# Performance work log

Hardware: AMD Instinct MI355X
Metric: run time of the kernel (lower is better)

## Reference

```python
import jax, jax.numpy as jnp
import numpy as np

N, C, H, W = 4, 256, 32, 32
NH = 2                      # att_nhead
HD = C // NH                # 128 per-head dim
MAX_DIS = 7
WS = 2 * MAX_DIS + 1        # 15 window side
WW = WS * WS                # 225 window positions
T = (C / NH) ** 0.5


def _gather_idx(h, w):
    # idx[wpos, m]: flat index into zero-padded (h+14, w+14) grid of the
    # neighbor at window offset wpos for query pixel m (== F.unfold semantics)
    pw = w + 2 * MAX_DIS
    dy, dx = np.meshgrid(np.arange(WS), np.arange(WS), indexing='ij')
    ys, xs = np.meshgrid(np.arange(h), np.arange(w), indexing='ij')
    idx = (dy.reshape(-1, 1) + ys.reshape(1, -1)) * pw + (dx.reshape(-1, 1) + xs.reshape(1, -1))
    return jnp.asarray(idx, dtype=jnp.int32)  # [WW, h*w]


def setup_inputs() -> dict:
    key = jax.random.key(0)
    ks = jax.random.split(key, 14)
    s = 0.02
    return {
        'q': jax.random.normal(ks[0], (N, C, H, W), jnp.float32),
        'k': jax.random.normal(ks[1], (N, C, H, W), jnp.float32),
        'v': jax.random.normal(ks[2], (N, C, H, W), jnp.float32),
        'Wq': jax.random.normal(ks[3], (C, C), jnp.float32) * s,
        'bq': jnp.zeros((C,), jnp.float32),
        'Wk': jax.random.normal(ks[4], (C, C), jnp.float32) * s,
        'bk': jnp.zeros((C,), jnp.float32),
        'Wv': jax.random.normal(ks[5], (C, C), jnp.float32) * s,
        'bv': jnp.zeros((C,), jnp.float32),
        'Wrel': jax.random.normal(ks[6], (NH, WW, HD), jnp.float32) * s,   # grouped 1x1 conv
        'brel': jnp.zeros((NH * WW,), jnp.float32),
        'V_bias': jax.random.normal(ks[7], (NH, HD, WW), jnp.float32) * s,
        'Wfc': jax.random.normal(ks[8], (C, C), jnp.float32) * s,
        'bfc': jnp.zeros((C,), jnp.float32),
    }


def _conv1x1(x, Wt, b):
    return jnp.einsum('nchw,dc->ndhw', x, Wt) + b[None, :, None, None]


def reference(q, k, v, Wq, bq, Wk, bk, Wv, bv, Wrel, brel, V_bias, Wfc, bfc):
    n, c, h, w = q.shape
    hw = h * w
    idx = _gather_idx(h, w)                                   # [WW, hw]
    pad = ((0, 0), (0, 0), (0, 0), (MAX_DIS, MAX_DIS), (MAX_DIS, MAX_DIS))

    q = _conv1x1(q, Wq, bq)
    k = _conv1x1(k, Wk, bk)
    v = _conv1x1(v, Wv, bv)

    # grouped 1x1 conv: relative position logits, [n, NH, WW, hw]
    rel = jnp.einsum('ngcxy,gwc->ngwxy', q.reshape(n, NH, HD, h, w), Wrel)
    rel = rel + brel.reshape(NH, WW)[None, :, :, None, None]
    rel = rel.reshape(n, NH, WW, hw)

    qs = (q / T).reshape(n, NH, HD, hw)

    # unfold K via zero-pad + gather: [n, NH, HD, WW, hw]
    k_pad = jnp.pad(k.reshape(n, NH, HD, h, w), pad).reshape(n, NH, HD, -1)
    k_un = k_pad[..., idx]
    qk = jnp.einsum('ngcm,ngcwm->ngwm', qs, k_un) + rel

    # boundary mask: neighbor inside the original image
    valid = jnp.pad(jnp.ones((h, w), jnp.float32), MAX_DIS).reshape(-1)[idx] > 0
    qk = jnp.where(valid[None, None], qk, jnp.float32(-1e8))
    attn = jax.nn.softmax(qk, axis=2)                         # over window positions

    agg_bias = jnp.einsum('ngwm,gcw->mngc', attn, V_bias).reshape(hw, n, c)

    # local2global scatter + dense einsum == gather of zero-padded V
    v_pad = jnp.pad(v.reshape(n, NH, HD, h, w), pad).reshape(n, NH, HD, -1)
    v_un = v_pad[..., idx]                                    # [n, NH, HD, WW, hw]
    agg_value = jnp.einsum('ngwm,ngcwm->mngc', attn, v_un).reshape(hw, n, c)

    out = (agg_value + agg_bias) @ Wfc.T + bfc                # [hw, n, c]
    return out
```

## Files before the change

### kernel.cpp

```cpp
#include <hip/hip_runtime.h>
#include <math.h>


typedef __attribute__((ext_vector_type(8))) short short8;
typedef __attribute__((ext_vector_type(4))) short short4v;
typedef __attribute__((ext_vector_type(4))) float floatx4;

__device__ __forceinline__ short f2bf(float f) {
    unsigned u = __float_as_uint(f);
    unsigned r = (u + 0x7fffu + ((u >> 16) & 1u)) >> 16;
    return (short)r;
}
__device__ __forceinline__ float bf2f(short s) {
    return __uint_as_float(((unsigned)(unsigned short)s) << 16);
}

__global__ __launch_bounds__(64)
void conv_w(const float* __restrict__ Wq, const float* __restrict__ Wk,
            const float* __restrict__ Wv, const float* __restrict__ Wfc,
            const float* __restrict__ Wrel, const float* __restrict__ Vb,
            short* __restrict__ Whi, short* __restrict__ Wlo,
            short* __restrict__ Wrh, short* __restrict__ Wrl,
            short* __restrict__ Vbh, short* __restrict__ Vbl)
{
    const int lane = threadIdx.x;
    const int n16 = lane & 15, quad = lane >> 4;
    const int z = blockIdx.z;

    if (z < 4) {
        const float* W = (z == 0 ? Wq : z == 1 ? Wk : z == 2 ? Wv : Wfc);
        const int dt = blockIdx.x, kc = blockIdx.y;
        const int d = dt * 16 + n16, cb = kc * 32 + quad * 8;
        float4 w0 = *(const float4*)&W[d * 256 + cb];
        float4 w1 = *(const float4*)&W[d * 256 + cb + 4];
        float f[8] = {w0.x, w0.y, w0.z, w0.w, w1.x, w1.y, w1.z, w1.w};
        short8 h8, l8;
#pragma unroll
        for (int j = 0; j < 8; ++j) {
            short hb = f2bf(f[j]);
            h8[j] = hb;
            l8[j] = f2bf(f[j] - bf2f(hb));
        }
        long off = (long)z * 65536 + (((long)(dt * 8 + kc) * 64) + lane) * 8;
        *(short8*)(Whi + off) = h8;
        *(short8*)(Wlo + off) = l8;
    } else if (z < 6) {
        const int g = z - 4;
        const int wt = blockIdx.x, kc = blockIdx.y;
        if (wt >= 15 || kc >= 4) return;
        const int w = wt * 16 + n16;
        const int cb = kc * 32 + quad * 8;
        float f[8] = {0.f, 0.f, 0.f, 0.f, 0.f, 0.f, 0.f, 0.f};
        if (w < 225) {
            float4 w0 = *(const float4*)&Wrel[(long)(g * 225 + w) * 128 + cb];
            float4 w1 = *(const float4*)&Wrel[(long)(g * 225 + w) * 128 + cb + 4];
            f[0] = w0.x; f[1] = w0.y; f[2] = w0.z; f[3] = w0.w;
            f[4] = w1.x; f[5] = w1.y; f[6] = w1.z; f[7] = w1.w;
        }
        short8 h8, l8;
#pragma unroll
        for (int j = 0; j < 8; ++j) {
            short hb = f2bf(f[j]);
            h8[j] = hb;
            l8[j] = f2bf(f[j] - bf2f(hb));
        }
        long off = (long)g * 30720 + (((long)(wt * 4 + kc) * 64) + lane) * 8;
        *(short8*)(Wrh + off) = h8;
        *(short8*)(Wrl + off) = l8;
    } else {
        const int g = z - 6;
        const int dt = blockIdx.x, wk = blockIdx.y;
        if (dt >= 8) return;
        const int ch = dt * 16 + n16;
        const int w0 = wk * 32 + quad * 8;
        float f[8];
#pragma unroll
        for (int j = 0; j < 8; ++j) {
            int w = w0 + j;
            f[j] = (w < 225) ? Vb[(long)(g * 128 + ch) * 225 + w] : 0.f;
        }
        short8 h8, l8;
#pragma unroll
        for (int j = 0; j < 8; ++j) {
            short hb = f2bf(f[j]);
            h8[j] = hb;
            l8[j] = f2bf(f[j] - bf2f(hb));
        }
        long off = (((long)(g * 128 + ch)) << 8) + w0;
        *(short8*)(Vbh + off) = h8;
        *(short8*)(Vbl + off) = l8;
    }
}

__global__ __launch_bounds__(256)
void mfma_proj(const float* __restrict__ q, const float* __restrict__ k,
               const float* __restrict__ v,
               const short* __restrict__ Whi, const short* __restrict__ Wlo,
               const float* __restrict__ bq, const float* __restrict__ bk,
               const float* __restrict__ bv,
               short* __restrict__ qhi, short* __restrict__ qlo,
               short* __restrict__ khi, short* __restrict__ klo,
               short* __restrict__ vhi, short* __restrict__ vlo)
{
    __shared__ float st[256 * 17];
    const int tid = threadIdx.x;
    const int wave = tid >> 6, lane = tid & 63;
    const int n16 = lane & 15, quad = lane >> 4;
    const int mt16 = blockIdx.x, z = blockIdx.y;
    const int sel = z >> 2, batch = z & 3;

    const float* X = (sel == 0 ? q : sel == 1 ? k : v) + ((long)batch << 18);

    {
        const float* src = X + ((long)tid << 10) + mt16 * 16;
        float4 a0 = *(const float4*)(src);
        float4 a1 = *(const float4*)(src + 4);
        float4 a2 = *(const float4*)(src + 8);
        float4 a3 = *(const float4*)(src + 12);
        float* d = &st[tid * 17];
        d[0] = a0.x; d[1] = a0.y; d[2] = a0.z; d[3] = a0.w;
        d[4] = a1.x; d[5] = a1.y; d[6] = a1.z; d[7] = a1.w;
        d[8] = a2.x; d[9] = a2.y; d[10] = a2.z; d[11] = a2.w;
        d[12] = a3.x; d[13] = a3.y; d[14] = a3.z; d[15] = a3.w;
    }

    const float* bias = (sel == 0 ? bq : sel == 1 ? bk : bv);
    float bbv[4][4];
#pragma unroll
    for (int i = 0; i < 4; ++i) {
        float4 b4 = *(const float4*)&bias[(wave * 4 + i) * 16 + quad * 4];
        bbv[i][0] = b4.x; bbv[i][1] = b4.y; bbv[i][2] = b4.z; bbv[i][3] = b4.w;
    }
    __syncthreads();

    floatx4 acc[4] = {{0.f,0.f,0.f,0.f},{0.f,0.f,0.f,0.f},
                      {0.f,0.f,0.f,0.f},{0.f,0.f,0.f,0.f}};
    const long abase = (long)sel * 65536 + (long)lane * 8;
#pragma unroll
    for (int kc = 0; kc < 8; ++kc) {
        short8 bh, bl;
        const float* col = &st[(kc * 32 + quad * 8) * 17 + n16];
#pragma unroll
        for (int j = 0; j < 8; ++j) {
            float f = col[j * 17];
            short hb = f2bf(f);
            bh[j] = hb;
            bl[j] = f2bf(f - bf2f(hb));
        }
#pragma unroll
        for (int i = 0; i < 4; ++i) {
            const int dt = wave * 4 + i;
            short8 ahi = *(const short8*)(Whi + abase + (long)(dt * 8 + kc) * 512);
            short8 alo = *(const short8*)(Wlo + abase + (long)(dt * 8 + kc) * 512);
            acc[i] = __builtin_amdgcn_mfma_f32_16x16x32_bf16(ahi, bh, acc[i], 0, 0, 0);
            acc[i] = __builtin_amdgcn_mfma_f32_16x16x32_bf16(ahi, bl, acc[i], 0, 0, 0);
            acc[i] = __builtin_amdgcn_mfma_f32_16x16x32_bf16(alo, bh, acc[i], 0, 0, 0);
        }
    }

    if (sel == 2) {
        const int m = mt16 * 16 + n16;
        const int yq = m >> 5, col = (m & 31) + 8;
#pragma unroll
        for (int i = 0; i < 4; ++i) {
            const int dt = wave * 4 + i;
#pragma unroll
            for (int r = 0; r < 4; ++r) {
                const int ch = dt * 16 + quad * 4 + r;
                const int gg = ch >> 7, chh = ch & 127;
                float f = acc[i][r] + bbv[i][r];
                short hb = f2bf(f);
                short lb = f2bf(f - bf2f(hb));
                long o = (((long)((batch * 2 + gg) * 128 + chh) * 32 + yq)) * 48 + col;
                vhi[o] = hb;
                vlo[o] = lb;
            }
        }
        {
            const int prow = mt16 >> 1, side = mt16 & 1;
            const int gg = tid >> 7, chp = tid & 127;
            long po = (((long)((batch * 2 + gg) * 128 + chp) * 32 + prow)) * 48 + side * 40;
            short8 zz = {0,0,0,0,0,0,0,0};
            *(short8*)(vhi + po) = zz;
            *(short8*)(vlo + po) = zz;
        }
        return;
    }

    __syncthreads();
    float* tile = st;
#pragma unroll
    for (int i = 0; i < 4; ++i) {
        const int dt = wave * 4 + i;
#pragma unroll
        for (int r = 0; r < 4; ++r)
            tile[n16 * 257 + dt * 16 + quad * 4 + r] = acc[i][r] + bbv[i][r];
    }
    __syncthreads();

    const float scale = (sel == 1) ? 0.08838834764831845f : 1.0f;
    const int m_l = tid >> 4, c16 = (tid & 15) * 16;
    const int m = mt16 * 16 + m_l;
    short* oh = sel ? khi : qhi;
    short* ol = sel ? klo : qlo;
#pragma unroll
    for (int half = 0; half < 2; ++half) {
        const int cg = c16 + half * 8;
        short8 h8, l8;
#pragma unroll
        for (int j = 0; j < 8; ++j) {
            float f = tile[m_l * 257 + cg + j] * scale;
            short hb = f2bf(f);
            h8[j] = hb;
            l8[j] = f2bf(f - bf2f(hb));
        }
        const int g = cg >> 7, ch = cg & 127;
        const long base = (((long)(batch * 2 + g) << 10) + m) * 128 + ch;
        *(short8*)(oh + base) = h8;
        *(short8*)(ol + base) = l8;
    }
}

__global__ __launch_bounds__(256)
void scores_pv(const short* __restrict__ qhi, const short* __restrict__ qlo,
               const short* __restrict__ khi, const short* __restrict__ klo,
               const short* __restrict__ Wrh, const short* __restrict__ Wrl,
               const float* __restrict__ brel,
               const short* __restrict__ vhi, const short* __restrict__ vlo,
               const short* __restrict__ Vbh, const short* __restrict__ Vbl,
               short* __restrict__ AGhi, short* __restrict__ AGlo)
{
    __shared__ __align__(16) float qk[16 * 241];
    __shared__ __align__(16) short pah[16 * 264];
    __shared__ __align__(16) short pal[16 * 264];
    __shared__ float invl[16];

    const int tid = threadIdx.x;
    const int wave = tid >> 6, lane = tid & 63;
    const int lin = blockIdx.x;
    const int bz  = lin & 7;
    const int yy  = lin >> 3;
    const int y   = yy >> 1;
    const int xt  = yy & 1;
    const int g = bz & 1;
    const int x0 = xt * 16;

    const int n16 = lane & 15, quad = lane >> 4;
    const long qbase = (((long)bz << 10) + y * 32 + x0 + n16) * 128 + quad * 8;
    short8 a_hi[4], a_lo[4];
#pragma unroll
    for (int ch = 0; ch < 4; ++ch) {
        a_hi[ch] = *(const short8*)(qhi + qbase + ch * 32);
        a_lo[ch] = *(const short8*)(qlo + qbase + ch * 32);
    }

    for (int wt = wave; wt < 15; wt += 4) {
        const short* Ah = Wrh + (long)g * 30720 + ((long)(wt * 4) * 64 + lane) * 8;
        const short* Al = Wrl + (long)g * 30720 + ((long)(wt * 4) * 64 + lane) * 8;
        floatx4 racc = {0.f, 0.f, 0.f, 0.f};
#pragma unroll
        for (int kc = 0; kc < 4; ++kc) {
            short8 whh = *(const short8*)(Ah + kc * 512);
            short8 wll = *(const short8*)(Al + kc * 512);
            racc = __builtin_amdgcn_mfma_f32_16x16x32_bf16(whh, a_hi[kc], racc, 0, 0, 0);
            racc = __builtin_amdgcn_mfma_f32_16x16x32_bf16(whh, a_lo[kc], racc, 0, 0, 0);
            racc = __builtin_amdgcn_mfma_f32_16x16x32_bf16(wll, a_hi[kc], racc, 0, 0, 0);
        }
#pragma unroll
        for (int r = 0; r < 4; ++r) {
            int w = wt * 16 + quad * 4 + r;
            if (w < 225) {
                int dy = w / 15, dx = w - dy * 15;
                qk[n16 * 241 + dy * 16 + dx] = racc[r] + brel[g * 225 + w];
            }
        }
    }
    __syncthreads();

    for (int e = tid; e < 16 * 241; e += 256) {
        int px = e / 241, idx = e - px * 241;
        int dy = idx >> 4, dx = idx & 15;
        int hy = y + dy - 7, hx = x0 + px + dx - 7;
        bool valid = (dx < 15) && (dy < 15) &&
                     (hy >= 0) && (hy < 32) && (hx >= 0) && (hx < 32);
        if (!valid) qk[e] = -1e8f;
    }
    __syncthreads();

    for (int dy = wave; dy < 15; dy += 4) {
        const int ky = y + dy - 7;
        if (ky < 0 || ky > 31) continue;
#pragma unroll
        for (int kxt = 0; kxt < 2; ++kxt) {
            const int kxg = x0 - 8 + kxt * 16 + n16;
            const long kb = (((long)bz << 10) + ky * 32 + kxg) * 128 + quad * 8;
            floatx4 acc = {0.f, 0.f, 0.f, 0.f};
#pragma unroll
            for (int ch = 0; ch < 4; ++ch) {
                short8 b_hi = *(const short8*)(khi + kb + ch * 32);
                short8 b_lo = *(const short8*)(klo + kb + ch * 32);
                acc = __builtin_amdgcn_mfma_f32_16x16x32_bf16(a_hi[ch], b_hi, acc, 0, 0, 0);
                acc = __builtin_amdgcn_mfma_f32_16x16x32_bf16(a_hi[ch], b_lo, acc, 0, 0, 0);
                acc = __builtin_amdgcn_mfma_f32_16x16x32_bf16(a_lo[ch], b_hi, acc, 0, 0, 0);
            }
            if (kxg >= 0 && kxg < 32) {
#pragma unroll
                for (int r = 0; r < 4; ++r) {
                    int m = quad * 4 + r;
                    int dx = kxg - (x0 + m) + 7;
                    if (dx >= 0 && dx < 15) {
                        int s = m * 241 + dy * 16 + dx;
                        qk[s] = qk[s] + acc[r];
                    }
                }
            }
        }
    }
    __syncthreads();

    {
        int px = tid >> 4, s = tid & 15;
        float mx = -3.0e38f;
        for (int w = s; w < 240; w += 16) mx = fmaxf(mx, qk[px * 241 + w]);
#pragma unroll
        for (int msk = 8; msk; msk >>= 1) mx = fmaxf(mx, __shfl_xor(mx, msk));
        float sum = 0.f;
        for (int w = s; w < 240; w += 16) {
            float p = __expf(qk[px * 241 + w] - mx);
            qk[px * 241 + w] = p;
            sum += p;
        }
#pragma unroll
        for (int msk = 8; msk; msk >>= 1) sum += __shfl_xor(sum, msk);
        if (s == 0) invl[px] = 1.0f / sum;
    }
    __syncthreads();

    for (int e = tid; e < 4096; e += 256) {
        int px = e >> 8, w = e & 255;
        float p = 0.f;
        if (w < 225) {
            int dy2 = w / 15, dx2 = w - dy2 * 15;
            p = qk[px * 241 + dy2 * 16 + dx2] * invl[px];
        }
        short hb = f2bf(p);
        pah[px * 264 + w] = hb;
        pal[px * 264 + w] = f2bf(p - bf2f(hb));
    }
    __syncthreads();

    floatx4 acc[2] = {{0.f,0.f,0.f,0.f},{0.f,0.f,0.f,0.f}};
    const int ch0a = (wave * 2) * 16;
    const int ch0b = (wave * 2 + 1) * 16;

#pragma unroll
    for (int wk = 0; wk < 8; ++wk) {
        short8 pa_h = *(const short8*)&pah[n16 * 264 + wk * 32 + quad * 8];
        short8 pa_l = *(const short8*)&pal[n16 * 264 + wk * 32 + quad * 8];
        const long vb0 = (((long)(g * 128 + ch0a + n16)) << 8) + wk * 32 + quad * 8;
        const long vb1 = (((long)(g * 128 + ch0b + n16)) << 8) + wk * 32 + quad * 8;
        short8 b0h = *(const short8*)(Vbh + vb0);
        short8 b0l = *(const short8*)(Vbl + vb0);
        short8 b1h = *(const short8*)(Vbh + vb1);
        short8 b1l = *(const short8*)(Vbl + vb1);
        acc[0] = __builtin_amdgcn_mfma_f32_16x16x32_bf16(pa_h, b0h, acc[0], 0, 0, 0);
        acc[0] = __builtin_amdgcn_mfma_f32_16x16x32_bf16(pa_h, b0l, acc[0], 0, 0, 0);
        acc[0] = __builtin_amdgcn_mfma_f32_16x16x32_bf16(pa_l, b0h, acc[0], 0, 0, 0);
        acc[1] = __builtin_amdgcn_mfma_f32_16x16x32_bf16(pa_h, b1h, acc[1], 0, 0, 0);
        acc[1] = __builtin_amdgcn_mfma_f32_16x16x32_bf16(pa_h, b1l, acc[1], 0, 0, 0);
        acc[1] = __builtin_amdgcn_mfma_f32_16x16x32_bf16(pa_l, b1h, acc[1], 0, 0, 0);
    }

    for (int dy = 0; dy < 15; ++dy) {
        const int ky = y + dy - 7;
        if (ky < 0 || ky > 31) continue;
        short8 bnd_h, bnd_l;
        const int rowoff = n16 * 264 + dy * 15 - n16 - 1;
#pragma unroll
        for (int j = 0; j < 8; ++j) {
            int kk = quad * 8 + j;
            int dx = kk - n16 - 1;
            bool valid = (unsigned)dx < 15u;
            int idx = valid ? (rowoff + kk) : 0;
            short vh = pah[idx];
            short vl = pal[idx];
            bnd_h[j] = valid ? vh : (short)0;
            bnd_l[j] = valid ? vl : (short)0;
        }
        const long v0o = (((long)((bz * 128 + ch0a + n16)) * 32 + ky)) * 48 + x0 + quad * 8;
        const long v1o = (((long)((bz * 128 + ch0b + n16)) * 32 + ky)) * 48 + x0 + quad * 8;
        short8 v0h = *(const short8*)(vhi + v0o);
        short8 v0l = *(const short8*)(vlo + v0o);
        short8 v1h = *(const short8*)(vhi + v1o);
        short8 v1l = *(const short8*)(vlo + v1o);
        acc[0] = __builtin_amdgcn_mfma_f32_16x16x32_bf16(bnd_h, v0h, acc[0], 0, 0, 0);
        acc[0] = __builtin_amdgcn_mfma_f32_16x16x32_bf16(bnd_h, v0l, acc[0], 0, 0, 0);
        acc[0] = __builtin_amdgcn_mfma_f32_16x16x32_bf16(bnd_l, v0h, acc[0], 0, 0, 0);
        acc[1] = __builtin_amdgcn_mfma_f32_16x16x32_bf16(bnd_h, v1h, acc[1], 0, 0, 0);
        acc[1] = __builtin_amdgcn_mfma_f32_16x16x32_bf16(bnd_h, v1l, acc[1], 0, 0, 0);
        acc[1] = __builtin_amdgcn_mfma_f32_16x16x32_bf16(bnd_l, v1h, acc[1], 0, 0, 0);
    }

    float* tile = qk;
#pragma unroll
    for (int t = 0; t < 2; ++t) {
        const int cb = (wave * 2 + t) * 16 + n16;
#pragma unroll
        for (int r = 0; r < 4; ++r)
            tile[(quad * 4 + r) * 133 + cb] = acc[t][r];
    }
    __syncthreads();

    const int sub = tid >> 6;
    short8 h8, l8;
#pragma unroll
    for (int j = 0; j < 8; ++j) {
        float f = tile[n16 * 133 + sub * 32 + quad * 8 + j];
        short hb = f2bf(f);
        h8[j] = hb;
        l8[j] = f2bf(f - bf2f(hb));
    }
    const int n = bz >> 1;
    const int mt16 = y * 2 + xt;
    const int kc = g * 4 + sub;
    long off = (long)n * 262144 + (((long)(mt16 * 8 + kc) * 64) + lane) * 8;
    *(short8*)(AGhi + off) = h8;
    *(short8*)(AGlo + off) = l8;
}

__global__ __launch_bounds__(256)
void mfma_fc(const short* __restrict__ Ahi, const short* __restrict__ Alo,
             const short* __restrict__ Whi, const short* __restrict__ Wlo,
             const float* __restrict__ bfc, float* __restrict__ out)
{
    __shared__ float tile[16 * 132];
    const int tid = threadIdx.x;
    const int wave = tid >> 6, lane = tid & 63;
    const int n16 = lane & 15, quad = lane >> 4;
    const int mt16 = blockIdx.x, db2 = blockIdx.y, nz = blockIdx.z;
    const int dt0 = db2 * 8 + wave * 2;

    const short* Bh = Ahi + (long)nz * 262144;
    const short* Bl = Alo + (long)nz * 262144;
    const long abase = (long)3 * 65536 + (long)lane * 8;

    float bbv[2][4];
#pragma unroll
    for (int p = 0; p < 2; ++p) {
        float4 b4 = *(const float4*)&bfc[(dt0 + p) * 16 + quad * 4];
        bbv[p][0] = b4.x; bbv[p][1] = b4.y; bbv[p][2] = b4.z; bbv[p][3] = b4.w;
    }

    floatx4 acc[2] = {{0.f,0.f,0.f,0.f},{0.f,0.f,0.f,0.f}};
#pragma unroll
    for (int kc = 0; kc < 8; ++kc) {
        const long bo = (long)(mt16 * 8 + kc) * 512 + (long)lane * 8;
        short8 bh = *(const short8*)(Bh + bo);
        short8 bl = *(const short8*)(Bl + bo);
#pragma unroll
        for (int p = 0; p < 2; ++p) {
            const int dt = dt0 + p;
            short8 ahi = *(const short8*)(Whi + abase + (long)(dt * 8 + kc) * 512);
            short8 alo = *(const short8*)(Wlo + abase + (long)(dt * 8 + kc) * 512);
            acc[p] = __builtin_amdgcn_mfma_f32_16x16x32_bf16(ahi, bh, acc[p], 0, 0, 0);
            acc[p] = __builtin_amdgcn_mfma_f32_16x16x32_bf16(ahi, bl, acc[p], 0, 0, 0);
            acc[p] = __builtin_amdgcn_mfma_f32_16x16x32_bf16(alo, bh, acc[p], 0, 0, 0);
        }
    }

#pragma unroll
    for (int p = 0; p < 2; ++p) {
        const int dl = (wave * 2 + p) * 16 + quad * 4;
#pragma unroll
        for (int r = 0; r < 4; ++r)
            tile[n16 * 132 + dl + r] = acc[p][r] + bbv[p][r];
    }
    __syncthreads();

    const int m_l = tid >> 4, d8 = (tid & 15) * 8;
    float4 o0 = *(const float4*)&tile[m_l * 132 + d8];
    float4 o1 = *(const float4*)&tile[m_l * 132 + d8 + 4];
    long ob = (long)(mt16 * 16 + m_l) * 1024 + nz * 256 + db2 * 128 + d8;
    *(float4*)&out[ob] = o0;
    *(float4*)&out[ob + 4] = o1;
}

extern "C" void kernel_launch(void* const* d_in, const int* in_sizes, int n_in,
                              void* d_out, int out_size, void* d_ws, size_t ws_size,
                              hipStream_t stream)
{
    const float* q    = (const float*)d_in[0];
    const float* k    = (const float*)d_in[1];
    const float* v    = (const float*)d_in[2];
    const float* Wq   = (const float*)d_in[3];
    const float* bq   = (const float*)d_in[4];
    const float* Wk   = (const float*)d_in[5];
    const float* bk   = (const float*)d_in[6];
    const float* Wv   = (const float*)d_in[7];
    const float* bv   = (const float*)d_in[8];
    const float* Wrel = (const float*)d_in[9];
    const float* brel = (const float*)d_in[10];
    const float* Vb   = (const float*)d_in[11];
    const float* Wfc  = (const float*)d_in[12];
    const float* bfc  = (const float*)d_in[13];
    float* out = (float*)d_out;

    float* ws   = (float*)d_ws;
    short* vhi  = (short*)(ws + 2097152);
    short* vlo  = (short*)(ws + 2883584);
    short* Vbh  = (short*)(ws + 4718592);
    short* Vbl  = (short*)(ws + 4751360);
    short* qhi  = (short*)(ws + 6561792);
    short* qlo  = (short*)(ws + 7086080);
    short* khi  = (short*)(ws + 7610368);
    short* klo  = (short*)(ws + 8134656);
    short* Whi  = (short*)(ws + 11804672);
    short* Wlo  = (short*)(ws + 11935744);
    short* AGhi = (short*)(ws + 12066816);
    short* AGlo = (short*)(ws + 12591104);
    short* Wrh  = (short*)(ws + 13115392);
    short* Wrl  = (short*)(ws + 13146112);

    conv_w<<<dim3(16, 8, 8), dim3(64), 0, stream>>>(Wq, Wk, Wv, Wfc, Wrel, Vb,
                                                    Whi, Wlo, Wrh, Wrl, Vbh, Vbl);

    mfma_proj<<<dim3(64, 12), dim3(256), 0, stream>>>(q, k, v, Whi, Wlo,
                                                      bq, bk, bv,
                                                      qhi, qlo, khi, klo,
                                                      vhi, vlo);

    scores_pv<<<dim3(512), dim3(256), 0, stream>>>(qhi, qlo, khi, klo,
                                                   Wrh, Wrl, brel,
                                                   vhi, vlo, Vbh, Vbl,
                                                   AGhi, AGlo);

    mfma_fc<<<dim3(64, 2, 4), dim3(256), 0, stream>>>(AGhi, AGlo, Whi, Wlo,
                                                      bfc, out);
}
```

Before: 162.4 us.

## Fold output projection into V and V_bias, drop separate FC kernel

Precomputes Wfc·Wv per head (and Wfc·V_bias, Wfc·bv) in a prep kernel, so the V projection directly produces per-head output-space values. The attention kernel then writes final outputs through atomicAdd across the two heads, which removes the AG intermediate buffer and the separate FC GEMM launch. In exchange, the V projection and V buffers double in size (256 channels per head), scores_pv moves to 512 threads, and the output needs a memset plus float atomics whose summation order is non-deterministic.

```diff
diff --git a/kernel.cpp b/kernel.cpp
--- a/kernel.cpp
+++ b/kernel.cpp
@@ -3,7 +3,6 @@
 
 
 typedef __attribute__((ext_vector_type(8))) short short8;
-typedef __attribute__((ext_vector_type(4))) short short4v;
 typedef __attribute__((ext_vector_type(4))) float floatx4;
 
 __device__ __forceinline__ short f2bf(float f) {
@@ -15,24 +14,129 @@
     return __uint_as_float(((unsigned)(unsigned short)s) << 16);
 }
 
-__global__ __launch_bounds__(64)
-void conv_w(const float* __restrict__ Wq, const float* __restrict__ Wk,
-            const float* __restrict__ Wv, const float* __restrict__ Wfc,
-            const float* __restrict__ Wrel, const float* __restrict__ Vb,
-            short* __restrict__ Whi, short* __restrict__ Wlo,
-            short* __restrict__ Wrh, short* __restrict__ Wrl,
-            short* __restrict__ Vbh, short* __restrict__ Vbl)
+__global__ __launch_bounds__(256)
+void prep(const float* __restrict__ Wq, const float* __restrict__ Wk,
+          const float* __restrict__ Wv, const float* __restrict__ Wfc,
+          const float* __restrict__ Wrel, const float* __restrict__ Vb,
+          const float* __restrict__ bv,
+          short* __restrict__ Whi, short* __restrict__ Wlo,
+          short* __restrict__ Wrh, short* __restrict__ Wrl,
+          short* __restrict__ Vbh, short* __restrict__ Vbl,
+          float* __restrict__ bcw)
 {
-    const int lane = threadIdx.x;
-    const int n16 = lane & 15, quad = lane >> 4;
-    const int z = blockIdx.z;
-
-    if (z < 4) {
-        const float* W = (z == 0 ? Wq : z == 1 ? Wk : z == 2 ? Wv : Wfc);
-        const int dt = blockIdx.x, kc = blockIdx.y;
+    __shared__ float wfc[16 * 128];
+    __shared__ float patch[16 * 257];
+    const int tid = threadIdx.x;
+    const int u = blockIdx.x;
+
+    if (u < 64) {
+        const bool isWc = (u < 32);
+        const int t = isWc ? u : u - 32;
+        const int g = t >> 4, dt = t & 15;
+        const int gs = g * 128;
+        {
+            int row = tid >> 4, ch8 = (tid & 15) * 8;
+            const float* src = &Wfc[(long)(dt * 16 + row) * 256 + gs + ch8];
+            float4 a = *(const float4*)src;
+            float4 b = *(const float4*)(src + 4);
+            float* d = &wfc[row * 128 + ch8];
+            d[0] = a.x; d[1] = a.y; d[2] = a.z; d[3] = a.w;
+            d[4] = b.x; d[5] = b.y; d[6] = b.z; d[7] = b.w;
+        }
+        __syncthreads();
+
+        const int dl = tid >> 4, c16 = (tid & 15) * 16;
+        float acc[16];
+#pragma unroll
+        for (int i = 0; i < 16; ++i) acc[i] = 0.f;
+
+        if (isWc) {
+            for (int ch = 0; ch < 128; ++ch) {
+                float wf = wfc[dl * 128 + ch];
+                const float* wr = &Wv[(long)(gs + ch) * 256 + c16];
+                float4 a = *(const float4*)wr;
+                float4 b = *(const float4*)(wr + 4);
+                float4 c = *(const float4*)(wr + 8);
+                float4 d4 = *(const float4*)(wr + 12);
+                acc[0] += wf * a.x;  acc[1] += wf * a.y;
+                acc[2] += wf * a.z;  acc[3] += wf * a.w;
+                acc[4] += wf * b.x;  acc[5] += wf * b.y;
+                acc[6] += wf * b.z;  acc[7] += wf * b.w;
+                acc[8] += wf * c.x;  acc[9] += wf * c.y;
+                acc[10] += wf * c.z; acc[11] += wf * c.w;
+                acc[12] += wf * d4.x; acc[13] += wf * d4.y;
+                acc[14] += wf * d4.z; acc[15] += wf * d4.w;
+            }
+#pragma unroll
+            for (int i = 0; i < 16; ++i) patch[dl * 257 + c16 + i] = acc[i];
+            if (tid < 16) {
+                float s = 0.f;
+                for (int ch = 0; ch < 128; ++ch)
+                    s += wfc[tid * 128 + ch] * bv[gs + ch];
+                bcw[g * 256 + dt * 16 + tid] = s;
+            }
+            __syncthreads();
+#pragma unroll
+            for (int s2 = 0; s2 < 2; ++s2) {
+                int idx = tid * 2 + s2;
+                int kc = idx >> 6, lane = idx & 63;
+                int n16 = lane & 15, quad = lane >> 4;
+                short8 h8, l8;
+#pragma unroll
+                for (int j = 0; j < 8; ++j) {
+                    float f = patch[n16 * 257 + kc * 32 + quad * 8 + j];
+                    short hb = f2bf(f);
+                    h8[j] = hb;
+                    l8[j] = f2bf(f - bf2f(hb));
+                }
+                long off = (long)(2 + g) * 65536 + (((long)(dt * 8 + kc) * 64) + lane) * 8;
+                *(short8*)(Whi + off) = h8;
+                *(short8*)(Wlo + off) = l8;
+            }
+        } else {
+            const int w16 = c16;
+            for (int ch = 0; ch < 128; ++ch) {
+                float wf = wfc[dl * 128 + ch];
+                const float* vr = &Vb[(long)(gs + ch) * 225];
+                if (w16 <= 208) {
+#pragma unroll
+                    for (int i = 0; i < 16; ++i) acc[i] += wf * vr[w16 + i];
+                } else {
+#pragma unroll
+                    for (int i = 0; i < 16; ++i) {
+                        int w = w16 + i;
+                        float vv = 0.f;
+                        if (w < 225) vv = vr[w];
+                        acc[i] += wf * vv;
+                    }
+                }
+            }
+            const long rb = (((long)(g * 256 + dt * 16 + dl)) << 8) + w16;
+#pragma unroll
+            for (int h = 0; h < 2; ++h) {
+                short8 h8, l8;
+#pragma unroll
+                for (int j = 0; j < 8; ++j) {
+                    float f = acc[h * 8 + j];
+                    short hb = f2bf(f);
+                    h8[j] = hb;
+                    l8[j] = f2bf(f - bf2f(hb));
+                }
+                *(short8*)(Vbh + rb + h * 8) = h8;
+                *(short8*)(Vbl + rb + h * 8) = l8;
+            }
+        }
+    } else if (u < 128) {
+        const int t = u - 64;
+        const int w = t >> 5, rem = t & 31;
+        const int dt = rem >> 1, kcq = (rem & 1) * 4;
+        const int sub = tid >> 6, lane = tid & 63;
+        const int kc = kcq + sub;
+        const int n16 = lane & 15, quad = lane >> 4;
+        const float* W = w ? Wk : Wq;
         const int d = dt * 16 + n16, cb = kc * 32 + quad * 8;
-        float4 w0 = *(const float4*)&W[d * 256 + cb];
-        float4 w1 = *(const float4*)&W[d * 256 + cb + 4];
+        float4 w0 = *(const float4*)&W[(long)d * 256 + cb];
+        float4 w1 = *(const float4*)&W[(long)d * 256 + cb + 4];
         float f[8] = {w0.x, w0.y, w0.z, w0.w, w1.x, w1.y, w1.z, w1.w};
         short8 h8, l8;
 #pragma unroll
@@ -41,13 +145,14 @@
             h8[j] = hb;
             l8[j] = f2bf(f[j] - bf2f(hb));
         }
-        long off = (long)z * 65536 + (((long)(dt * 8 + kc) * 64) + lane) * 8;
+        long off = (long)w * 65536 + (((long)(dt * 8 + kc) * 64) + lane) * 8;
         *(short8*)(Whi + off) = h8;
         *(short8*)(Wlo + off) = l8;
-    } else if (z < 6) {
-        const int g = z - 4;
-        const int wt = blockIdx.x, kc = blockIdx.y;
-        if (wt >= 15 || kc >= 4) return;
+    } else {
+        const int t = u - 128;
+        const int g = t / 15, wt = t - g * 15;
+        const int kc = tid >> 6, lane = tid & 63;
+        const int n16 = lane & 15, quad = lane >> 4;
         const int w = wt * 16 + n16;
         const int cb = kc * 32 + quad * 8;
         float f[8] = {0.f, 0.f, 0.f, 0.f, 0.f, 0.f, 0.f, 0.f};
@@ -67,28 +172,6 @@
         long off = (long)g * 30720 + (((long)(wt * 4 + kc) * 64) + lane) * 8;
         *(short8*)(Wrh + off) = h8;
         *(short8*)(Wrl + off) = l8;
-    } else {
-        const int g = z - 6;
-        const int dt = blockIdx.x, wk = blockIdx.y;
-        if (dt >= 8) return;
-        const int ch = dt * 16 + n16;
-        const int w0 = wk * 32 + quad * 8;
-        float f[8];
-#pragma unroll
-        for (int j = 0; j < 8; ++j) {
-            int w = w0 + j;
-            f[j] = (w < 225) ? Vb[(long)(g * 128 + ch) * 225 + w] : 0.f;
-        }
-        short8 h8, l8;
-#pragma unroll
-        for (int j = 0; j < 8; ++j) {
-            short hb = f2bf(f[j]);
-            h8[j] = hb;
-            l8[j] = f2bf(f[j] - bf2f(hb));
-        }
-        long off = (((long)(g * 128 + ch)) << 8) + w0;
-        *(short8*)(Vbh + off) = h8;
-        *(short8*)(Vbl + off) = l8;
     }
 }
 
@@ -97,7 +180,7 @@
                const float* __restrict__ v,
                const short* __restrict__ Whi, const short* __restrict__ Wlo,
                const float* __restrict__ bq, const float* __restrict__ bk,
-               const float* __restrict__ bv,
+               const float* __restrict__ bcw,
                short* __restrict__ qhi, short* __restrict__ qlo,
                short* __restrict__ khi, short* __restrict__ klo,
                short* __restrict__ vhi, short* __restrict__ vlo)
@@ -124,7 +207,7 @@
         d[12] = a3.x; d[13] = a3.y; d[14] = a3.z; d[15] = a3.w;
     }
 
-    const float* bias = (sel == 0 ? bq : sel == 1 ? bk : bv);
+    const float* bias = (sel == 0) ? bq : (sel == 1) ? bk : (bcw + (sel - 2) * 256);
     float bbv[4][4];
 #pragma unroll
     for (int i = 0; i < 4; ++i) {
@@ -158,35 +241,6 @@
         }
     }
 
-    if (sel == 2) {
-        const int m = mt16 * 16 + n16;
-        const int yq = m >> 5, col = (m & 31) + 8;
-#pragma unroll
-        for (int i = 0; i < 4; ++i) {
-            const int dt = wave * 4 + i;
-#pragma unroll
-            for (int r = 0; r < 4; ++r) {
-                const int ch = dt * 16 + quad * 4 + r;
-                const int gg = ch >> 7, chh = ch & 127;
-                float f = acc[i][r] + bbv[i][r];
-                short hb = f2bf(f);
-                short lb = f2bf(f - bf2f(hb));
-                long o = (((long)((batch * 2 + gg) * 128 + chh) * 32 + yq)) * 48 + col;
-                vhi[o] = hb;
-                vlo[o] = lb;
-            }
-        }
-        {
-            const int prow = mt16 >> 1, side = mt16 & 1;
-            const int gg = tid >> 7, chp = tid & 127;
-            long po = (((long)((batch * 2 + gg) * 128 + chp) * 32 + prow)) * 48 + side * 40;
-            short8 zz = {0,0,0,0,0,0,0,0};
-            *(short8*)(vhi + po) = zz;
-            *(short8*)(vlo + po) = zz;
-        }
-        return;
-    }
-
     __syncthreads();
     float* tile = st;
 #pragma unroll
@@ -197,6 +251,31 @@
             tile[n16 * 257 + dt * 16 + quad * 4 + r] = acc[i][r] + bbv[i][r];
     }
     __syncthreads();
+
+    if (sel >= 2) {
+        const int g = sel - 2;
+        const int yq = mt16 >> 1, xb = (mt16 & 1) * 16;
+        short8 h0, h1, l0, l1;
+#pragma unroll
+        for (int j = 0; j < 8; ++j) {
+            float f0 = tile[j * 257 + tid];
+            float f1 = tile[(j + 8) * 257 + tid];
+            short hb0 = f2bf(f0), hb1 = f2bf(f1);
+            h0[j] = hb0; l0[j] = f2bf(f0 - bf2f(hb0));
+            h1[j] = hb1; l1[j] = f2bf(f1 - bf2f(hb1));
+        }
+        long o = ((long)((batch * 2 + g) * 256 + tid) * 32 + yq) * 48 + 8 + xb;
+        *(short8*)(vhi + o) = h0;
+        *(short8*)(vhi + o + 8) = h1;
+        *(short8*)(vlo + o) = l0;
+        *(short8*)(vlo + o + 8) = l1;
+        const int prow = mt16 >> 1, side = mt16 & 1;
+        long po = ((long)((batch * 2 + g) * 256 + tid) * 32 + prow) * 48 + side * 40;
+        short8 zz = {0,0,0,0,0,0,0,0};
+        *(short8*)(vhi + po) = zz;
+        *(short8*)(vlo + po) = zz;
+        return;
+    }
 
     const float scale = (sel == 1) ? 0.08838834764831845f : 1.0f;
     const int m_l = tid >> 4, c16 = (tid & 15) * 16;
@@ -221,14 +300,14 @@
     }
 }
 
-__global__ __launch_bounds__(256)
+__global__ __launch_bounds__(512)
 void scores_pv(const short* __restrict__ qhi, const short* __restrict__ qlo,
                const short* __restrict__ khi, const short* __restrict__ klo,
                const short* __restrict__ Wrh, const short* __restrict__ Wrl,
                const float* __restrict__ brel,
                const short* __restrict__ vhi, const short* __restrict__ vlo,
                const short* __restrict__ Vbh, const short* __restrict__ Vbl,
-               short* __restrict__ AGhi, short* __restrict__ AGlo)
+               const float* __restrict__ bfc, float* __restrict__ out)
 {
     __shared__ __align__(16) float qk[16 * 241];
     __shared__ __align__(16) short pah[16 * 264];
@@ -254,7 +333,7 @@
         a_lo[ch] = *(const short8*)(qlo + qbase + ch * 32);
     }
 
-    for (int wt = wave; wt < 15; wt += 4) {
+    for (int wt = wave; wt < 15; wt += 8) {
         const short* Ah = Wrh + (long)g * 30720 + ((long)(wt * 4) * 64 + lane) * 8;
         const short* Al = Wrl + (long)g * 30720 + ((long)(wt * 4) * 64 + lane) * 8;
         floatx4 racc = {0.f, 0.f, 0.f, 0.f};
@@ -277,7 +356,7 @@
     }
     __syncthreads();
 
-    for (int e = tid; e < 16 * 241; e += 256) {
+    for (int e = tid; e < 16 * 241; e += 512) {
         int px = e / 241, idx = e - px * 241;
         int dy = idx >> 4, dx = idx & 15;
         int hy = y + dy - 7, hx = x0 + px + dx - 7;
@@ -287,7 +366,7 @@
     }
     __syncthreads();
 
-    for (int dy = wave; dy < 15; dy += 4) {
+    for (int dy = wave; dy < 15; dy += 8) {
         const int ky = y + dy - 7;
         if (ky < 0 || ky > 31) continue;
 #pragma unroll
@@ -319,24 +398,24 @@
     __syncthreads();
 
     {
-        int px = tid >> 4, s = tid & 15;
+        int px = tid >> 5, s = tid & 31;
         float mx = -3.0e38f;
-        for (int w = s; w < 240; w += 16) mx = fmaxf(mx, qk[px * 241 + w]);
-#pragma unroll
-        for (int msk = 8; msk; msk >>= 1) mx = fmaxf(mx, __shfl_xor(mx, msk));
+        for (int w = s; w < 240; w += 32) mx = fmaxf(mx, qk[px * 241 + w]);
+#pragma unroll
+        for (int msk = 16; msk; msk >>= 1) mx = fmaxf(mx, __shfl_xor(mx, msk));
         float sum = 0.f;
-        for (int w = s; w < 240; w += 16) {
+        for (int w = s; w < 240; w += 32) {
             float p = __expf(qk[px * 241 + w] - mx);
             qk[px * 241 + w] = p;
             sum += p;
         }
 #pragma unroll
-        for (int msk = 8; msk; msk >>= 1) sum += __shfl_xor(sum, msk);
+        for (int msk = 16; msk; msk >>= 1) sum += __shfl_xor(sum, msk);
         if (s == 0) invl[px] = 1.0f / sum;
     }
     __syncthreads();
 
-    for (int e = tid; e < 4096; e += 256) {
+    for (int e = tid; e < 4096; e += 512) {
         int px = e >> 8, w = e & 255;
         float p = 0.f;
         if (w < 225) {
@@ -350,15 +429,15 @@
     __syncthreads();
 
     floatx4 acc[2] = {{0.f,0.f,0.f,0.f},{0.f,0.f,0.f,0.f}};
-    const int ch0a = (wave * 2) * 16;
-    const int ch0b = (wave * 2 + 1) * 16;
+    const int ch0a = wave * 32;
+    const int ch0b = wave * 32 + 16;
 
 #pragma unroll
     for (int wk = 0; wk < 8; ++wk) {
         short8 pa_h = *(const short8*)&pah[n16 * 264 + wk * 32 + quad * 8];
         short8 pa_l = *(const short8*)&pal[n16 * 264 + wk * 32 + quad * 8];
-        const long vb0 = (((long)(g * 128 + ch0a + n16)) << 8) + wk * 32 + quad * 8;
-        const long vb1 = (((long)(g * 128 + ch0b + n16)) << 8) + wk * 32 + quad * 8;
+        const long vb0 = (((long)(g * 256 + ch0a + n16)) << 8) + wk * 32 + quad * 8;
+        const long vb1 = (((long)(g * 256 + ch0b + n16)) << 8) + wk * 32 + quad * 8;
         short8 b0h = *(const short8*)(Vbh + vb0);
         short8 b0l = *(const short8*)(Vbl + vb0);
         short8 b1h = *(const short8*)(Vbh + vb1);
@@ -387,8 +466,8 @@
             bnd_h[j] = valid ? vh : (short)0;
             bnd_l[j] = valid ? vl : (short)0;
         }
-        const long v0o = (((long)((bz * 128 + ch0a + n16)) * 32 + ky)) * 48 + x0 + quad * 8;
-        const long v1o = (((long)((bz * 128 + ch0b + n16)) * 32 + ky)) * 48 + x0 + quad * 8;
+        const long v0o = (((long)(bz * 256 + ch0a + n16)) * 32 + ky) * 48 + x0 + quad * 8;
+        const long v1o = (((long)(bz * 256 + ch0b + n16)) * 32 + ky) * 48 + x0 + quad * 8;
         short8 v0h = *(const short8*)(vhi + v0o);
         short8 v0l = *(const short8*)(vlo + v0o);
         short8 v1h = *(const short8*)(vhi + v1o);
@@ -401,88 +480,18 @@
         acc[1] = __builtin_amdgcn_mfma_f32_16x16x32_bf16(bnd_l, v1h, acc[1], 0, 0, 0);
     }
 
-    float* tile = qk;
+    const int n = bz >> 1;
 #pragma unroll
     for (int t = 0; t < 2; ++t) {
-        const int cb = (wave * 2 + t) * 16 + n16;
-#pragma unroll
-        for (int r = 0; r < 4; ++r)
-            tile[(quad * 4 + r) * 133 + cb] = acc[t][r];
-    }
-    __syncthreads();
-
-    const int sub = tid >> 6;
-    short8 h8, l8;
-#pragma unroll
-    for (int j = 0; j < 8; ++j) {
-        float f = tile[n16 * 133 + sub * 32 + quad * 8 + j];
-        short hb = f2bf(f);
-        h8[j] = hb;
-        l8[j] = f2bf(f - bf2f(hb));
-    }
-    const int n = bz >> 1;
-    const int mt16 = y * 2 + xt;
-    const int kc = g * 4 + sub;
-    long off = (long)n * 262144 + (((long)(mt16 * 8 + kc) * 64) + lane) * 8;
-    *(short8*)(AGhi + off) = h8;
-    *(short8*)(AGlo + off) = l8;
-}
-
-__global__ __launch_bounds__(256)
-void mfma_fc(const short* __restrict__ Ahi, const short* __restrict__ Alo,
-             const short* __restrict__ Whi, const short* __restrict__ Wlo,
-             const float* __restrict__ bfc, float* __restrict__ out)
-{
-    __shared__ float tile[16 * 132];
-    const int tid = threadIdx.x;
-    const int wave = tid >> 6, lane = tid & 63;
-    const int n16 = lane & 15, quad = lane >> 4;
-    const int mt16 = blockIdx.x, db2 = blockIdx.y, nz = blockIdx.z;
-    const int dt0 = db2 * 8 + wave * 2;
-
-    const short* Bh = Ahi + (long)nz * 262144;
-    const short* Bl = Alo + (long)nz * 262144;
-    const long abase = (long)3 * 65536 + (long)lane * 8;
-
-    float bbv[2][4];
-#pragma unroll
-    for (int p = 0; p < 2; ++p) {
-        float4 b4 = *(const float4*)&bfc[(dt0 + p) * 16 + quad * 4];
-        bbv[p][0] = b4.x; bbv[p][1] = b4.y; bbv[p][2] = b4.z; bbv[p][3] = b4.w;
-    }
-
-    floatx4 acc[2] = {{0.f,0.f,0.f,0.f},{0.f,0.f,0.f,0.f}};
-#pragma unroll
-    for (int kc = 0; kc < 8; ++kc) {
-        const long bo = (long)(mt16 * 8 + kc) * 512 + (long)lane * 8;
-        short8 bh = *(const short8*)(Bh + bo);
-        short8 bl = *(const short8*)(Bl + bo);
-#pragma unroll
-        for (int p = 0; p < 2; ++p) {
-            const int dt = dt0 + p;
-            short8 ahi = *(const short8*)(Whi + abase + (long)(dt * 8 + kc) * 512);
-            short8 alo = *(const short8*)(Wlo + abase + (long)(dt * 8 + kc) * 512);
-            acc[p] = __builtin_amdgcn_mfma_f32_16x16x32_bf16(ahi, bh, acc[p], 0, 0, 0);
-            acc[p] = __builtin_amdgcn_mfma_f32_16x16x32_bf16(ahi, bl, acc[p], 0, 0, 0);
-            acc[p] = __builtin_amdgcn_mfma_f32_16x16x32_bf16(alo, bh, acc[p], 0, 0, 0);
-        }
-    }
-
-#pragma unroll
-    for (int p = 0; p < 2; ++p) {
-        const int dl = (wave * 2 + p) * 16 + quad * 4;
-#pragma unroll
-        for (int r = 0; r < 4; ++r)
-            tile[n16 * 132 + dl + r] = acc[p][r] + bbv[p][r];
-    }
-    __syncthreads();
-
-    const int m_l = tid >> 4, d8 = (tid & 15) * 8;
-    float4 o0 = *(const float4*)&tile[m_l * 132 + d8];
-    float4 o1 = *(const float4*)&tile[m_l * 132 + d8 + 4];
-    long ob = (long)(mt16 * 16 + m_l) * 1024 + nz * 256 + db2 * 128 + d8;
-    *(float4*)&out[ob] = o0;
-    *(float4*)&out[ob + 4] = o1;
+        const int d = (t ? ch0b : ch0a) + n16;
+        const float badd = (g == 0) ? bfc[d] : 0.f;
+#pragma unroll
+        for (int r = 0; r < 4; ++r) {
+            const int px = quad * 4 + r;
+            long o = ((long)(y * 32 + x0 + px) * 4 + n) * 256 + d;
+            atomicAdd(&out[o], acc[t][r] + badd);
+        }
+    }
 }
 
 extern "C" void kernel_launch(void* const* d_in, const int* in_sizes, int n_in,
@@ -507,33 +516,31 @@
 
     float* ws   = (float*)d_ws;
     short* vhi  = (short*)(ws + 2097152);
-    short* vlo  = (short*)(ws + 2883584);
-    short* Vbh  = (short*)(ws + 4718592);
-    short* Vbl  = (short*)(ws + 4751360);
+    short* vlo  = (short*)(ws + 3670016);
+    short* Vbh  = (short*)(ws + 5242880);
+    short* Vbl  = (short*)(ws + 5308416);
+    float* bcw  = ws + 5373952;
     short* qhi  = (short*)(ws + 6561792);
     short* qlo  = (short*)(ws + 7086080);
     short* khi  = (short*)(ws + 7610368);
     short* klo  = (short*)(ws + 8134656);
     short* Whi  = (short*)(ws + 11804672);
     short* Wlo  = (short*)(ws + 11935744);
-    short* AGhi = (short*)(ws + 12066816);
-    short* AGlo = (short*)(ws + 12591104);
     short* Wrh  = (short*)(ws + 13115392);
     short* Wrl  = (short*)(ws + 13146112);
 
-    conv_w<<<dim3(16, 8, 8), dim3(64), 0, stream>>>(Wq, Wk, Wv, Wfc, Wrel, Vb,
-                                                    Whi, Wlo, Wrh, Wrl, Vbh, Vbl);
-
-    mfma_proj<<<dim3(64, 12), dim3(256), 0, stream>>>(q, k, v, Whi, Wlo,
-                                                      bq, bk, bv,
+    hipMemsetAsync(d_out, 0, out_size, stream);
+
+    prep<<<dim3(158), dim3(256), 0, stream>>>(Wq, Wk, Wv, Wfc, Wrel, Vb, bv,
+                                              Whi, Wlo, Wrh, Wrl, Vbh, Vbl, bcw);
+
+    mfma_proj<<<dim3(64, 16), dim3(256), 0, stream>>>(q, k, v, Whi, Wlo,
+                                                      bq, bk, bcw,
                                                       qhi, qlo, khi, klo,
                                                       vhi, vlo);
 
-    scores_pv<<<dim3(512), dim3(256), 0, stream>>>(qhi, qlo, khi, klo,
+    scores_pv<<<dim3(512), dim3(512), 0, stream>>>(qhi, qlo, khi, klo,
                                                    Wrh, Wrl, brel,
                                                    vhi, vlo, Vbh, Vbl,
-                                                   AGhi, AGlo);
-
-    mfma_fc<<<dim3(64, 2, 4), dim3(256), 0, stream>>>(AGhi, AGlo, Whi, Wlo,
-                                                      bfc, out);
+                                                   bfc, out);
 }
```

Result: slower. 262.1 us (+61.4%).
